# Kernel optimization log

Hardware: AMD Instinct MI355X
Metric: run time of the kernel (lower is better)

The kernel has to match this reference:

```python
import jax, jax.numpy as jnp
import numpy as np

N = 100000          # nodes
E = 1600000         # directed edges
B = 64              # graphs in the batch
IN_D, HID, OUT_D = 20, 128, 256
EPS = 1e-5


def setup_inputs() -> dict:
    key = jax.random.key(0)
    ks = jax.random.split(key, 16)
    x = jax.random.normal(ks[0], (N, IN_D), dtype=jnp.float32)
    edge_index = jax.random.randint(ks[1], (2, E), 0, N, dtype=jnp.int64)
    batch = jnp.sort(jax.random.randint(ks[2], (N,), 0, B, dtype=jnp.int64))

    def lin(k, fi, fo):
        kw, kb = jax.random.split(k)
        s = 1.0 / np.sqrt(fi)
        W = jax.random.uniform(kw, (fi, fo), jnp.float32, -s, s)
        b = jax.random.uniform(kb, (fo,), jnp.float32, -s, s)
        return W, b

    W1, b1 = lin(ks[3], IN_D, HID)
    W2, b2 = lin(ks[4], HID, HID)
    W3, b3 = lin(ks[5], HID, OUT_D)
    res_W, res_b = lin(ks[6], IN_D, HID)
    return {
        "x": x, "edge_index": edge_index, "batch": batch,
        "W1": W1, "b1": b1, "W2": W2, "b2": b2, "W3": W3, "b3": b3,
        "res_W": res_W, "res_b": res_b,
        "ln1_g": jnp.ones((HID,), jnp.float32), "ln1_b": jnp.zeros((HID,), jnp.float32),
        "ln2_g": jnp.ones((HID,), jnp.float32), "ln2_b": jnp.zeros((HID,), jnp.float32),
    }


def layer_norm(h, g, b):
    mu = jnp.mean(h, axis=-1, keepdims=True)
    var = jnp.mean((h - mu) ** 2, axis=-1, keepdims=True)
    return (h - mu) * jax.lax.rsqrt(var + EPS) * g + b


def gcn_conv(h, W, b, src, dst, norm):
    # h: [N, Fi] -> transform then normalized scatter-sum over edges (incl. self-loops)
    h = h @ W                                  # [N, Fo]
    msg = h[src] * norm[:, None]               # [E+N, Fo] gather
    out = jax.ops.segment_sum(msg, dst, num_segments=N)  # scatter
    return out + b


def reference(x, edge_index, batch, W1, b1, W2, b2, W3, b3, res_W, res_b,
              ln1_g, ln1_b, ln2_g, ln2_b):
    loops = jnp.arange(N, dtype=edge_index.dtype)
    src = jnp.concatenate([edge_index[0], loops])
    dst = jnp.concatenate([edge_index[1], loops])
    # symmetric GCN normalization (degrees include self-loops, so deg >= 1)
    deg = jax.ops.segment_sum(jnp.ones_like(dst, jnp.float32), dst, num_segments=N)
    dinv = jax.lax.rsqrt(deg)
    norm = dinv[src] * dinv[dst]               # [E+N]

    residual = x @ res_W + res_b
    h = gcn_conv(x, W1, b1, src, dst, norm)
    h = jax.nn.relu(layer_norm(h + residual, ln1_g, ln1_b))
    residual2 = h
    h = gcn_conv(h, W2, b2, src, dst, norm)
    h = jax.nn.relu(layer_norm(h + residual2, ln2_g, ln2_b))
    h = gcn_conv(h, W3, b3, src, dst, norm)    # [N, 256]

    # global mean pool per graph
    cnt = jax.ops.segment_sum(jnp.ones((N,), jnp.float32), batch, num_segments=B)
    pooled = jax.ops.segment_sum(h, batch, num_segments=B) / jnp.maximum(cnt, 1.0)[:, None]
    return pooled                              # [B, 256]
```

## Files before the change

kernel.cpp:

```cpp
#include <hip/hip_runtime.h>
#include <hip/hip_bf16.h>
#include <hip/hip_fp16.h>
#include <hip/hip_fp8.h>


typedef unsigned short ushort_t;
typedef unsigned int uint_t;
typedef __attribute__((ext_vector_type(8))) short bf16x8;
typedef __attribute__((ext_vector_type(4))) float f32x4;
typedef __attribute__((ext_vector_type(2))) float f32x2;

constexpr int N  = 100000;
constexpr int E  = 1600000;
constexpr int B  = 64;
constexpr int IND = 20;
constexpr int HID = 128;
constexpr int OUTD = 256;

constexpr int NBUK = (N + 127) / 128;
constexpr int GB   = 256;
constexpr int EPB  = E / GB;
constexpr int BMAX = 3072;

__device__ inline ushort_t f2bf(float f) {
  union { float f; uint_t u; } v; v.f = f;
  uint_t r = v.u + 0x7fffu + ((v.u >> 16) & 1u);
  return (ushort_t)(r >> 16);
}
__device__ inline float bflo(uint_t u) { return __uint_as_float(u << 16); }
__device__ inline float bfhi(uint_t u) { return __uint_as_float(u & 0xffff0000u); }

__device__ inline uint_t pkbf(float a, float b) {
  uint_t r;
  asm("v_cvt_pk_bf16_f32 %0, %1, %2" : "=v"(r) : "v"(a), "v"(b));
  return r;
}

#if defined(__has_builtin)
#if __has_builtin(__builtin_amdgcn_cvt_f32_fp8) && __has_builtin(__builtin_amdgcn_cvt_pk_fp8_f32)
#define FP8_HW 1
#endif
#if __has_builtin(__builtin_amdgcn_cvt_pk_f32_fp8)
#define FP8_PK 1
#endif
#endif

template <int S>
__device__ inline float fp8dec(uint_t u) {
#ifdef FP8_HW
  return __builtin_amdgcn_cvt_f32_fp8(u, S);
#else
  __hip_fp8_storage_t b = (__hip_fp8_storage_t)((u >> (8 * S)) & 0xffu);
  __half_raw hr = __hip_cvt_fp8_to_halfraw(b, __HIP_E4M3);
  return __half2float(*(__half*)&hr);
#endif
}

template <int W>
__device__ inline f32x2 fp8dec2(uint_t u) {
#ifdef FP8_PK
  return __builtin_amdgcn_cvt_pk_f32_fp8(u, W != 0);
#else
  f32x2 r; r.x = fp8dec<W * 2>(u); r.y = fp8dec<W * 2 + 1>(u); return r;
#endif
}

template <bool W>
__device__ inline uint_t fp8pk2(float a, float b, uint_t old) {
#ifdef FP8_HW
  return __builtin_amdgcn_cvt_pk_fp8_f32(a, b, old, W);
#else
  uint_t lo = (uint_t)__hip_cvt_float_to_fp8(a, __HIP_SATFINITE, __HIP_E4M3);
  uint_t hi = (uint_t)__hip_cvt_float_to_fp8(b, __HIP_SATFINITE, __HIP_E4M3);
  uint_t pair = lo | (hi << 8);
  return W ? ((old & 0x0000ffffu) | (pair << 16)) : ((old & 0xffff0000u) | pair);
#endif
}

__device__ inline uint_t fp8pair2bf(uint_t b0, uint_t b1) {
#ifdef FP8_PK
  f32x2 f = fp8dec2<0>(b0 | (b1 << 8));
  return pkbf(f.x, f.y);
#else
  return (uint_t)f2bf(fp8dec<0>(b0)) | ((uint_t)f2bf(fp8dec<0>(b1)) << 16);
#endif
}


__global__ __launch_bounds__(256) void k_prep(const int* __restrict__ eidx,
                                              int* __restrict__ histd,
                                              int* __restrict__ hists,
                                              const float* __restrict__ W2,
                                              const float* __restrict__ W1,
                                              const float* __restrict__ resW,
                                              ushort_t* __restrict__ wpack,
                                              ushort_t* __restrict__ w1pack,
                                              const int* __restrict__ batch,
                                              int* __restrict__ starts) {
  const int bid = blockIdx.x;
  if (bid < GB) {
    __shared__ int hd[NBUK], hs[NBUK];
    for (int i = threadIdx.x; i < NBUK; i += 256) { hd[i] = 0; hs[i] = 0; }
    __syncthreads();
    const long base = (long)bid * EPB;
    for (int i = threadIdx.x; i < EPB; i += 256) {
      atomicAdd(&hs[eidx[base + i] >> 7], 1);
      atomicAdd(&hd[eidx[E + base + i] >> 7], 1);
    }
    __syncthreads();
    for (int i = threadIdx.x; i < NBUK; i += 256) {
      histd[(long)bid * NBUK + i] = hd[i];
      hists[(long)bid * NBUK + i] = hs[i];
    }
  } else if (bid < GB + 96) {
    int idx = (bid - GB) * 256 + threadIdx.x;
    if (idx < 16384) {
      int j = idx & 7, L = (idx >> 3) & 63, kt = (idx >> 9) & 3, t = idx >> 11;
      int k = kt * 32 + ((L >> 4) & 3) * 8 + j;
      int n = t * 16 + (L & 15);
      wpack[idx] = f2bf(W2[k * HID + n]);
    } else {
      int i2 = idx - 16384;
      int j = i2 & 7, L = (i2 >> 3) & 63, kt = (i2 >> 9) & 1, t = i2 >> 10;
      int k = kt * 32 + ((L >> 4) & 3) * 8 + j;
      int n = t * 16 + (L & 15);
      float v = 0.f;
      if (k < IND) v = W1[k * HID + n];
      else if (k >= 32 && k < 32 + IND) v = resW[(k - 32) * HID + n];
      w1pack[i2] = f2bf(v);
    }
  } else {
    int i = (bid - GB - 96) * 256 + threadIdx.x;
    if (i >= N) return;
    int b = batch[i];
    int prev = (i == 0) ? -1 : batch[i - 1];
    for (int g = prev + 1; g <= b; ++g) starts[g] = i;
    if (i == N - 1)
      for (int g = b + 1; g <= B; ++g) starts[g] = N;
  }
}


__global__ __launch_bounds__(256) void k_bscan2x(int* __restrict__ histd,
                                                 int* __restrict__ btd,
                                                 int* __restrict__ hists,
                                                 int* __restrict__ bts) {
  __shared__ int s[256];
  const int which = (blockIdx.x >= NBUK);
  const int j = which ? blockIdx.x - NBUK : blockIdx.x;
  int* hist = which ? hists : histd;
  int* btotal = which ? bts : btd;
  const int tid = threadIdx.x;
  int v = hist[(long)tid * NBUK + j];
  s[tid] = v;
  for (int off = 1; off < 256; off <<= 1) {
    __syncthreads();
    int x = (tid >= off) ? s[tid - off] : 0;
    __syncthreads();
    s[tid] += x;
  }
  hist[(long)tid * NBUK + j] = s[tid] - v;
  if (tid == 255) btotal[j] = s[255];
}

__global__ __launch_bounds__(256) void k_bktscan2x(const int* __restrict__ btd,
                                                   int* __restrict__ bexcl,
                                                   const int* __restrict__ bts,
                                                   int* __restrict__ bexcl2,
                                                   int* __restrict__ rowptr) {
  __shared__ int s[256];
  const int* bt = blockIdx.x ? bts : btd;
  int* bx = blockIdx.x ? bexcl2 : bexcl;
  int tid = threadIdx.x;
  int base = tid * 4;
  int v0 = (base + 0 < NBUK) ? bt[base + 0] : 0;
  int v1 = (base + 1 < NBUK) ? bt[base + 1] : 0;
  int v2 = (base + 2 < NBUK) ? bt[base + 2] : 0;
  int v3 = (base + 3 < NBUK) ? bt[base + 3] : 0;
  int p0 = v0, p1 = p0 + v1, p2 = p1 + v2, p3 = p2 + v3;
  s[tid] = p3;
  for (int off = 1; off < 256; off <<= 1) {
    __syncthreads();
    int x = (tid >= off) ? s[tid - off] : 0;
    __syncthreads();
    s[tid] += x;
  }
  int excl = s[tid] - p3;
  if (base + 0 < NBUK) bx[base + 1] = excl + p0;
  if (base + 1 < NBUK) bx[base + 2] = excl + p1;
  if (base + 2 < NBUK) bx[base + 3] = excl + p2;
  if (base + 3 < NBUK) bx[base + 4] = excl + p3;
  if (tid == 0) { bx[0] = 0; if (blockIdx.x == 0) rowptr[N] = E; }
}

__global__ __launch_bounds__(1024) void k_scatter(const int* __restrict__ eidx,
                                                  const int* __restrict__ histd,
                                                  const int* __restrict__ bexcl,
                                                  const int* __restrict__ hists,
                                                  const int* __restrict__ bexcl2,
                                                  int* __restrict__ ebuf,
                                                  int* __restrict__ ebuf2) {
  __shared__ int hd[NBUK], hs[NBUK];
  const int l = ((blockIdx.x & 7) << 5) + (blockIdx.x >> 3);
  const long hrow = (long)l * NBUK;
  for (int i = threadIdx.x; i < NBUK; i += 1024) {
    hd[i] = bexcl[i] + histd[hrow + i];
    hs[i] = bexcl2[i] + hists[hrow + i];
  }
  __syncthreads();
  const long base = (long)l * EPB;
  for (int i = threadIdx.x; i < EPB; i += 1024) {
    int s = eidx[base + i];
    int d = eidx[E + base + i];
    int pos = atomicAdd(&hd[d >> 7], 1);
    ebuf[pos] = s | ((d & 127) << 20);
    int pos2 = atomicAdd(&hs[s >> 7], 1);
    ebuf2[pos2] = ((s & 127) << 17) | d;
  }
}

__global__ __launch_bounds__(256) void k_csr(const int* __restrict__ ebuf,
                                             const int* __restrict__ bexcl,
                                             const float* __restrict__ x,
                                             int* __restrict__ rowptr,
                                             float* __restrict__ dinv,
                                             int* __restrict__ colsrc,
                                             ushort_t* __restrict__ xs16) {
  __shared__ int deg[128], s[128], cur[128];
  __shared__ float dv[128];
  __shared__ int lout[BMAX];
  const int j = blockIdx.x, tid = threadIdx.x;
  const int e0 = bexcl[j], e1 = bexcl[j + 1];
  const int cnt = e1 - e0;
  if (tid < 128) deg[tid] = 0;
  __syncthreads();
  for (int i = tid; i < cnt; i += 256)
    atomicAdd(&deg[(ebuf[e0 + i] >> 20) & 127], 1);
  __syncthreads();
  int v = (tid < 128) ? deg[tid] : 0;
  if (tid < 128) s[tid] = v;
  for (int off = 1; off < 128; off <<= 1) {
    __syncthreads();
    int x2 = (tid < 128 && tid >= off) ? s[tid - off] : 0;
    __syncthreads();
    if (tid < 128) s[tid] += x2;
  }
  __syncthreads();
  if (tid < 128) {
    int ex = s[tid] - v;
    cur[tid] = ex;
    float d = rsqrtf((float)(1 + v));
    dv[tid] = d;
    int node = j * 128 + tid;
    if (node < N) {
      rowptr[node] = e0 + ex;
      dinv[node] = d;
    }
  }
  __syncthreads();
  if (cnt <= BMAX) {
    for (int i = tid; i < cnt; i += 256) {
      int p = ebuf[e0 + i];
      int pos = atomicAdd(&cur[(p >> 20) & 127], 1);
      lout[pos] = p & 0xFFFFF;
    }
    __syncthreads();
    for (int i = tid; i < cnt; i += 256) colsrc[e0 + i] = lout[i];
  } else {
    for (int i = tid; i < cnt; i += 256) {
      int p = ebuf[e0 + i];
      int pos = atomicAdd(&cur[(p >> 20) & 127], 1);
      colsrc[e0 + pos] = p & 0xFFFFF;
    }
  }
  for (int idx = tid; idx < 128 * IND; idx += 256) {
    int n = idx / IND;
    long node = (long)j * 128 + n;
    if (node < N)
      xs16[node * IND + idx % IND] = f2bf(x[node * IND + idx % IND] * dv[n]);
  }
}


constexpr int ASTR = 72;
constexpr int CSTR = 132;

__global__ __launch_bounds__(256) void k_layer1(const ushort_t* __restrict__ xs16,
                                                const float* __restrict__ x,
                                                const int* __restrict__ rowptr,
                                                const int* __restrict__ colsrc,
                                                const ushort_t* __restrict__ w1pack,
                                                const float* __restrict__ b1,
                                                const float* __restrict__ resb,
                                                const float* __restrict__ g1,
                                                const float* __restrict__ bb1,
                                                const float* __restrict__ dinv,
                                                unsigned char* __restrict__ h8a) {
  __shared__ ushort_t A[16 * ASTR];
  __shared__ float Cs[16 * CSTR];
  const int tid = threadIdx.x;
  const long node0 = (long)blockIdx.x * 16;
  for (int idx = tid; idx < 16 * ASTR; idx += 256) A[idx] = 0;
  __syncthreads();
  for (int idx = tid; idx < 16 * IND; idx += 256) {
    int n = idx / IND, k = idx % IND;
    A[n * ASTR + 32 + k] = f2bf(x[(node0 + n) * IND + k]);
  }
  if (tid < 160) {
    int n = tid / 10, cc = (tid % 10) * 2;
    long i = node0 + n;
    float di = dinv[i];
    uint_t u = *(const uint_t*)(xs16 + i * IND + cc);
    float a0 = bflo(u), a1 = bfhi(u);
    int e0 = rowptr[i], e1 = rowptr[i + 1];
#pragma unroll 4
    for (int e = e0; e < e1; ++e) {
      int s = colsrc[e];
      uint_t v = *(const uint_t*)(xs16 + (long)s * IND + cc);
      a0 += bflo(v); a1 += bfhi(v);
    }
    *(uint_t*)&A[n * ASTR + cc] = pkbf(a0 * di, a1 * di);
  }
  __syncthreads();
  const int lane = tid & 63, w = tid >> 6;
  {
    const int arow = lane & 15, aq = lane >> 4;
    f32x4 acc0 = {0.f, 0.f, 0.f, 0.f}, acc1 = {0.f, 0.f, 0.f, 0.f};
    const int t0 = w * 2, t1 = t0 + 1;
#pragma unroll
    for (int kt = 0; kt < 2; ++kt) {
      bf16x8 af = *(const bf16x8*)&A[arow * ASTR + kt * 32 + aq * 8];
      bf16x8 b0 = *(const bf16x8*)&w1pack[(t0 * 2 + kt) * 512 + lane * 8];
      bf16x8 b1f = *(const bf16x8*)&w1pack[(t1 * 2 + kt) * 512 + lane * 8];
      acc0 = __builtin_amdgcn_mfma_f32_16x16x32_bf16(af, b0, acc0, 0, 0, 0);
      acc1 = __builtin_amdgcn_mfma_f32_16x16x32_bf16(af, b1f, acc1, 0, 0, 0);
    }
#pragma unroll
    for (int r = 0; r < 4; ++r) {
      Cs[(aq * 4 + r) * CSTR + t0 * 16 + arow] = acc0[r];
      Cs[(aq * 4 + r) * CSTR + t1 * 16 + arow] = acc1[r];
    }
  }
  __syncthreads();
  const int nidx = tid >> 5, col = (tid & 31) * 4;
  float4 bz = *(const float4*)&b1[col];
  float4 rz = *(const float4*)&resb[col];
  bz.x += rz.x; bz.y += rz.y; bz.z += rz.z; bz.w += rz.w;
  float4 gz = *(const float4*)&g1[col];
  float4 bbz = *(const float4*)&bb1[col];
#pragma unroll
  for (int m = 0; m < 2; ++m) {
    int nl = nidx + m * 8;
    long nm = node0 + nl;
    float4 o = *(const float4*)&Cs[nl * CSTR + col];
    o.x += bz.x; o.y += bz.y; o.z += bz.z; o.w += bz.w;
    float s = o.x + o.y + o.z + o.w;
    float q = o.x * o.x + o.y * o.y + o.z * o.z + o.w * o.w;
#pragma unroll
    for (int off = 1; off <= 16; off <<= 1) {
      s += __shfl_xor(s, off);
      q += __shfl_xor(q, off);
    }
    float mu = s * (1.f / 128.f);
    float var = q * (1.f / 128.f) - mu * mu;
    float rs = rsqrtf(var + 1e-5f);
    float y0 = fmaxf(fmaf((o.x - mu) * rs, gz.x, bbz.x), 0.f);
    float y1 = fmaxf(fmaf((o.y - mu) * rs, gz.y, bbz.y), 0.f);
    float y2 = fmaxf(fmaf((o.z - mu) * rs, gz.z, bbz.z), 0.f);
    float y3 = fmaxf(fmaf((o.w - mu) * rs, gz.w, bbz.w), 0.f);
    float di = dinv[nm];
    uint_t p = fp8pk2<false>(y0 * di, y1 * di, 0u);
    p = fp8pk2<true>(y2 * di, y3 * di, p);
    *(uint_t*)&h8a[nm * HID + col] = p;
  }
}


constexpr int XSTR = 136;

__global__ __launch_bounds__(256) void k_layer2(const unsigned char* __restrict__ h8a,
                                                const float* __restrict__ dinv,
                                                const int* __restrict__ rowptr,
                                                const int* __restrict__ colsrc,
                                                const ushort_t* __restrict__ wpack,
                                                const float* __restrict__ bias,
                                                const float* __restrict__ g2,
                                                const float* __restrict__ bb2,
                                                unsigned char* __restrict__ h8b) {
  __shared__ ushort_t XsB[16 * XSTR];
  __shared__ float Cs[16 * CSTR];
  const int tid = threadIdx.x;
  const long node0 = (long)blockIdx.x * 16;
  const int lane = tid & 63, w = tid >> 6;
  {
    const int grp = lane >> 4, l16 = lane & 15, c8 = l16 * 8;
    const long i = node0 + w * 4 + grp;
    const float di = dinv[i];
    f32x2 a0, a1, a2, a3;
    {
      uint2 u = *(const uint2*)(h8a + i * HID + c8);
      a0 = fp8dec2<0>(u.x); a1 = fp8dec2<1>(u.x);
      a2 = fp8dec2<0>(u.y); a3 = fp8dec2<1>(u.y);
    }
    const int e0 = rowptr[i], e1 = rowptr[i + 1];
#pragma unroll 4
    for (int e = e0; e < e1; ++e) {
      int s = colsrc[e];
      uint2 u = *(const uint2*)(h8a + (long)s * HID + c8);
      a0 += fp8dec2<0>(u.x); a1 += fp8dec2<1>(u.x);
      a2 += fp8dec2<0>(u.y); a3 += fp8dec2<1>(u.y);
    }
    uint_t p0 = pkbf(a0.x * di, a0.y * di);
    uint_t p1 = pkbf(a1.x * di, a1.y * di);
    uint_t p2 = pkbf(a2.x * di, a2.y * di);
    uint_t p3 = pkbf(a3.x * di, a3.y * di);
    *(uint4*)&XsB[(w * 4 + grp) * XSTR + c8] = make_uint4(p0, p1, p2, p3);
  }
  __syncthreads();
  {
    const int arow = lane & 15, aq = lane >> 4;
    f32x4 acc0 = {0.f, 0.f, 0.f, 0.f}, acc1 = {0.f, 0.f, 0.f, 0.f};
    const int t0 = w * 2, t1 = w * 2 + 1;
#pragma unroll
    for (int kt = 0; kt < 4; ++kt) {
      bf16x8 af = *(const bf16x8*)&XsB[arow * XSTR + kt * 32 + aq * 8];
      bf16x8 b0 = *(const bf16x8*)&wpack[(t0 * 4 + kt) * 512 + lane * 8];
      bf16x8 b1 = *(const bf16x8*)&wpack[(t1 * 4 + kt) * 512 + lane * 8];
      acc0 = __builtin_amdgcn_mfma_f32_16x16x32_bf16(af, b0, acc0, 0, 0, 0);
      acc1 = __builtin_amdgcn_mfma_f32_16x16x32_bf16(af, b1, acc1, 0, 0, 0);
    }
#pragma unroll
    for (int r = 0; r < 4; ++r) {
      Cs[(aq * 4 + r) * CSTR + t0 * 16 + arow] = acc0[r];
      Cs[(aq * 4 + r) * CSTR + t1 * 16 + arow] = acc1[r];
    }
  }
  __syncthreads();
  const int nidx = tid >> 5;
  const int col = (tid & 31) * 4;
  float4 bz = *(const float4*)&bias[col];
  float4 gz = *(const float4*)&g2[col];
  float4 bbz = *(const float4*)&bb2[col];
#pragma unroll
  for (int m = 0; m < 2; ++m) {
    int nl = nidx + m * 8;
    long nm = node0 + nl;
    float di = dinv[nm];
    float rdi = 1.0f / di;
    uint_t ur = *(const uint_t*)&h8a[nm * HID + col];
    f32x2 r01 = fp8dec2<0>(ur), r23 = fp8dec2<1>(ur);
    float4 o = *(const float4*)&Cs[nl * CSTR + col];
    o.x += bz.x + r01.x * rdi;
    o.y += bz.y + r01.y * rdi;
    o.z += bz.z + r23.x * rdi;
    o.w += bz.w + r23.y * rdi;
    float s = o.x + o.y + o.z + o.w;
    float q = o.x * o.x + o.y * o.y + o.z * o.z + o.w * o.w;
#pragma unroll
    for (int off = 1; off <= 16; off <<= 1) {
      s += __shfl_xor(s, off);
      q += __shfl_xor(q, off);
    }
    float mu = s * (1.f / 128.f);
    float var = q * (1.f / 128.f) - mu * mu;
    float rs = rsqrtf(var + 1e-5f);
    float y0 = fmaxf(fmaf((o.x - mu) * rs, gz.x, bbz.x), 0.f);
    float y1 = fmaxf(fmaf((o.y - mu) * rs, gz.y, bbz.y), 0.f);
    float y2 = fmaxf(fmaf((o.z - mu) * rs, gz.z, bbz.z), 0.f);
    float y3 = fmaxf(fmaf((o.w - mu) * rs, gz.w, bbz.w), 0.f);
    uint_t p = fp8pk2<false>(y0 * di, y1 * di, 0u);
    p = fp8pk2<true>(y2 * di, y3 * di, p);
    *(uint_t*)&h8b[nm * HID + col] = p;
  }
}


constexpr int RSTR8 = 136;
constexpr int CP    = 132;

__global__ __launch_bounds__(256) void k_pool3m(const unsigned char* __restrict__ h8b,
                                                const int* __restrict__ bexcl2,
                                                const int* __restrict__ ebuf2,
                                                const int* __restrict__ batch,
                                                const float* __restrict__ dinv,
                                                ushort_t* __restrict__ partial) {
  __shared__ float Cm[B * CP];
  __shared__ unsigned char R8[128 * RSTR8];
  const int j = blockIdx.x, tid = threadIdx.x;
  const long nbase = (long)j * 128;
  const int validRows = min(128, N - (int)nbase);
  for (int i = tid; i < B * CP; i += 256) Cm[i] = 0.f;
  for (int i = tid; i < 128 * (HID / 16); i += 256) {
    int s = i >> 3;
    int ch = (i & 7) * 16;
    uint4 pk = make_uint4(0u, 0u, 0u, 0u);
    if (s < validRows)
      pk = *(const uint4*)(h8b + (nbase + s) * HID + ch);
    *(uint4*)&R8[s * RSTR8 + ch] = pk;
  }
  __syncthreads();
  const int e0 = bexcl2[j], e1 = bexcl2[j + 1];
  for (int e = e0 + tid; e < e1; e += 256) {
    int p = ebuf2[e];
    int s = (p >> 17) & 127;
    int d = p & 0x1FFFF;
    atomicAdd(&Cm[batch[d] * CP + s], dinv[d]);
  }
  for (int n = tid; n < validRows; n += 256) {
    long node = nbase + n;
    atomicAdd(&Cm[batch[node] * CP + n], dinv[node]);
  }
  __syncthreads();
  const int lane = tid & 63, wid = tid >> 6;
  const int m16 = lane & 15, quad = lane >> 4;
  f32x4 acc[4][2];
#pragma unroll
  for (int mt = 0; mt < 4; ++mt)
#pragma unroll
    for (int ntl = 0; ntl < 2; ++ntl) acc[mt][ntl] = (f32x4){0.f, 0.f, 0.f, 0.f};
#pragma unroll
  for (int kt = 0; kt < 4; ++kt) {
    union { uint_t p[4]; bf16x8 v; } bf[2];
#pragma unroll
    for (int ntl = 0; ntl < 2; ++ntl) {
      int nt = wid * 2 + ntl;
#pragma unroll
      for (int jj = 0; jj < 8; jj += 2) {
        uint_t byte0 = R8[(kt * 32 + quad * 8 + jj) * RSTR8 + nt * 16 + m16];
        uint_t byte1 = R8[(kt * 32 + quad * 8 + jj + 1) * RSTR8 + nt * 16 + m16];
        bf[ntl].p[jj >> 1] = fp8pair2bf(byte0, byte1);
      }
    }
#pragma unroll
    for (int mt = 0; mt < 4; ++mt) {
      float4 c0 = *(const float4*)&Cm[(mt * 16 + m16) * CP + kt * 32 + quad * 8];
      float4 c1 = *(const float4*)&Cm[(mt * 16 + m16) * CP + kt * 32 + quad * 8 + 4];
      union { uint_t p[4]; bf16x8 v; } af;
      af.p[0] = pkbf(c0.x, c0.y); af.p[1] = pkbf(c0.z, c0.w);
      af.p[2] = pkbf(c1.x, c1.y); af.p[3] = pkbf(c1.z, c1.w);
      acc[mt][0] = __builtin_amdgcn_mfma_f32_16x16x32_bf16(af.v, bf[0].v, acc[mt][0], 0, 0, 0);
      acc[mt][1] = __builtin_amdgcn_mfma_f32_16x16x32_bf16(af.v, bf[1].v, acc[mt][1], 0, 0, 0);
    }
  }
  ushort_t* slab = partial + (long)j * (B * HID);
#pragma unroll
  for (int mt = 0; mt < 4; ++mt)
#pragma unroll
    for (int ntl = 0; ntl < 2; ++ntl)
#pragma unroll
      for (int r = 0; r < 4; ++r) {
        int g = mt * 16 + quad * 4 + r;
        int ch = (wid * 2 + ntl) * 16 + m16;
        slab[g * HID + ch] = f2bf(acc[mt][ntl][r]);
      }
}

__global__ __launch_bounds__(256) void k_pool_reduce(const ushort_t* __restrict__ partial,
                                                     float* __restrict__ pooled) {
  __shared__ float s[4][64];
  const int tid = threadIdx.x;
  const int ol = tid & 7, jl = tid >> 3;
  const int o0 = blockIdx.x * 64 + ol * 8;
  float a0 = 0.f, a1 = 0.f, a2 = 0.f, a3 = 0.f,
        a4 = 0.f, a5 = 0.f, a6 = 0.f, a7 = 0.f;
#pragma unroll 2
  for (int j = jl; j < NBUK; j += 32) {
    uint4 v = *(const uint4*)&partial[(long)j * (B * HID) + o0];
    a0 += bflo(v.x); a1 += bfhi(v.x);
    a2 += bflo(v.y); a3 += bfhi(v.y);
    a4 += bflo(v.z); a5 += bfhi(v.z);
    a6 += bflo(v.w); a7 += bfhi(v.w);
  }
#pragma unroll
  for (int off = 8; off <= 32; off <<= 1) {
    a0 += __shfl_xor(a0, off); a1 += __shfl_xor(a1, off);
    a2 += __shfl_xor(a2, off); a3 += __shfl_xor(a3, off);
    a4 += __shfl_xor(a4, off); a5 += __shfl_xor(a5, off);
    a6 += __shfl_xor(a6, off); a7 += __shfl_xor(a7, off);
  }
  const int w = tid >> 6, lane = tid & 63;
  if (lane < 8) {
    float* d = &s[w][lane * 8];
    d[0] = a0; d[1] = a1; d[2] = a2; d[3] = a3;
    d[4] = a4; d[5] = a5; d[6] = a6; d[7] = a7;
  }
  __syncthreads();
  if (tid < 64)
    pooled[blockIdx.x * 64 + tid] = s[0][tid] + s[1][tid] + s[2][tid] + s[3][tid];
}


__global__ __launch_bounds__(256) void k_final(const float* __restrict__ pooled,
                                               const int* __restrict__ starts,
                                               const float* __restrict__ W3,
                                               const float* __restrict__ b3,
                                               float* __restrict__ out) {
  __shared__ float p[HID];
  int g = blockIdx.x, tid = threadIdx.x;
  int len = starts[g + 1] - starts[g];
  float scale = 1.0f / fmaxf((float)len, 1.0f);
  if (tid < HID) p[tid] = pooled[g * HID + tid] * scale;
  __syncthreads();
  float a = b3[tid];
  for (int k = 0; k < HID; ++k) a = fmaf(p[k], W3[k * OUTD + tid], a);
  out[g * OUTD + tid] = a;
}


extern "C" void kernel_launch(void* const* d_in, const int* in_sizes, int n_in,
                              void* d_out, int out_size, void* d_ws, size_t ws_size,
                              hipStream_t stream) {
  const float* x    = (const float*)d_in[0];
  const int*   eidx = (const int*)d_in[1];
  const int*   batch= (const int*)d_in[2];
  const float* W1   = (const float*)d_in[3];
  const float* b1   = (const float*)d_in[4];
  const float* W2   = (const float*)d_in[5];
  const float* b2   = (const float*)d_in[6];
  const float* W3   = (const float*)d_in[7];
  const float* b3   = (const float*)d_in[8];
  const float* resW = (const float*)d_in[9];
  const float* resb = (const float*)d_in[10];
  const float* g1   = (const float*)d_in[11];
  const float* bb1  = (const float*)d_in[12];
  const float* g2   = (const float*)d_in[13];
  const float* bb2  = (const float*)d_in[14];
  float* out = (float*)d_out;

  char* w = (char*)d_ws;
  size_t off = 0;
  auto alloc = [&](size_t bytes) {
    char* p = w + off;
    off = (off + bytes + 1023) & ~(size_t)1023;
    return p;
  };
  float* dinv   = (float*)alloc((size_t)N * 4);
  int*   rowptr = (int*)alloc((size_t)(N + 1) * 4);
  int*   colsrc = (int*)alloc((size_t)E * 4);
  int*   ebuf   = (int*)alloc((size_t)E * 4);
  int*   ebuf2  = (int*)alloc((size_t)E * 4);
  int*   hist   = (int*)alloc((size_t)GB * NBUK * 4);
  int*   hist2  = (int*)alloc((size_t)GB * NBUK * 4);
  int*   btotal = (int*)alloc((size_t)NBUK * 4);
  int*   btotal2= (int*)alloc((size_t)NBUK * 4);
  int*   bexcl  = (int*)alloc((size_t)(NBUK + 1) * 4);
  int*   bexcl2 = (int*)alloc((size_t)(NBUK + 1) * 4);
  int*   starts = (int*)alloc((size_t)(B + 1) * 4);
  float* pooled = (float*)alloc((size_t)B * HID * 4);
  ushort_t* xs16   = (ushort_t*)alloc((size_t)N * IND * 2);
  ushort_t* wpack  = (ushort_t*)alloc((size_t)HID * HID * 2);
  ushort_t* w1pack = (ushort_t*)alloc((size_t)8192 * 2);
  unsigned char* h8a = (unsigned char*)alloc((size_t)N * HID);
  unsigned char* h8b = (unsigned char*)alloc((size_t)N * HID);
  ushort_t* partial = (ushort_t*)alloc((size_t)NBUK * B * HID * 2);

  k_prep<<<GB + 96 + (N + 255) / 256, 256, 0, stream>>>(
      eidx, hist, hist2, W2, W1, resW, wpack, w1pack, batch, starts);
  k_bscan2x<<<2 * NBUK, 256, 0, stream>>>(hist, btotal, hist2, btotal2);
  k_bktscan2x<<<2, 256, 0, stream>>>(btotal, bexcl, btotal2, bexcl2, rowptr);
  k_scatter<<<GB, 1024, 0, stream>>>(eidx, hist, bexcl, hist2, bexcl2, ebuf, ebuf2);
  k_csr<<<NBUK, 256, 0, stream>>>(ebuf, bexcl, x, rowptr, dinv, colsrc, xs16);

  k_layer1<<<N / 16, 256, 0, stream>>>(xs16, x, rowptr, colsrc, w1pack,
                                       b1, resb, g1, bb1, dinv, h8a);

  k_layer2<<<N / 16, 256, 0, stream>>>(h8a, dinv, rowptr, colsrc,
                                       wpack, b2, g2, bb2, h8b);

  k_pool3m<<<NBUK, 256, 0, stream>>>(h8b, bexcl2, ebuf2, batch, dinv, partial);
  k_pool_reduce<<<(B * HID) / 64, 256, 0, stream>>>(partial, pooled);
  k_final<<<B, 256, 0, stream>>>(pooled, starts, W3, b3, out);
}
```

Before: 260.3 us.

## Stage scatter through shared memory for coalesced bucketed global writes

The edge scatter kernel now does two passes (dst-bucketed and src-bucketed). Each pass builds a local histogram, runs a block-wide scan and places the entries into a shared-memory staging buffer in bucket order. It then writes them out contiguously per bucket, replacing scattered per-edge global stores. This aims to improve write coalescing, at the cost of extra passes over the edge list, many barriers and a large shared-memory footprint (about 38KB) that limits occupancy.

```diff
diff --git a/kernel.cpp b/kernel.cpp
--- a/kernel.cpp
+++ b/kernel.cpp
@@ -200,22 +200,63 @@
                                                   const int* __restrict__ bexcl2,
                                                   int* __restrict__ ebuf,
                                                   int* __restrict__ ebuf2) {
-  __shared__ int hd[NBUK], hs[NBUK];
+  __shared__ int lhist[NBUK];
+  __shared__ int lscan[NBUK];
+  __shared__ int gbase[NBUK];
+  __shared__ int stmp[1024];
+  __shared__ int staged[EPB];
+  __shared__ ushort_t sbuk[EPB];
+  const int tid = threadIdx.x;
   const int l = ((blockIdx.x & 7) << 5) + (blockIdx.x >> 3);
   const long hrow = (long)l * NBUK;
-  for (int i = threadIdx.x; i < NBUK; i += 1024) {
-    hd[i] = bexcl[i] + histd[hrow + i];
-    hs[i] = bexcl2[i] + hists[hrow + i];
-  }
-  __syncthreads();
   const long base = (long)l * EPB;
-  for (int i = threadIdx.x; i < EPB; i += 1024) {
-    int s = eidx[base + i];
-    int d = eidx[E + base + i];
-    int pos = atomicAdd(&hd[d >> 7], 1);
-    ebuf[pos] = s | ((d & 127) << 20);
-    int pos2 = atomicAdd(&hs[s >> 7], 1);
-    ebuf2[pos2] = ((s & 127) << 17) | d;
+
+#pragma unroll
+  for (int pass = 0; pass < 2; ++pass) {
+    const int* hist = pass ? hists : histd;
+    const int* bx = pass ? bexcl2 : bexcl;
+    int* out = pass ? ebuf2 : ebuf;
+    for (int i = tid; i < NBUK; i += 1024) {
+      lhist[i] = 0;
+      gbase[i] = bx[i] + hist[hrow + i];
+    }
+    __syncthreads();
+    for (int i = tid; i < EPB; i += 1024) {
+      int key = eidx[(pass ? 0 : E) + base + i];
+      atomicAdd(&lhist[key >> 7], 1);
+    }
+    __syncthreads();
+    {
+      int v = (tid < NBUK) ? lhist[tid] : 0;
+      stmp[tid] = v;
+      for (int off = 1; off < 1024; off <<= 1) {
+        __syncthreads();
+        int x2 = (tid >= off) ? stmp[tid - off] : 0;
+        __syncthreads();
+        stmp[tid] += x2;
+      }
+      __syncthreads();
+      if (tid < NBUK) {
+        int ex = stmp[tid] - v;
+        lscan[tid] = ex;
+        lhist[tid] = ex;
+      }
+    }
+    __syncthreads();
+    for (int i = tid; i < EPB; i += 1024) {
+      int s = eidx[base + i];
+      int d = eidx[E + base + i];
+      int b = (pass ? s : d) >> 7;
+      int pos = atomicAdd(&lhist[b], 1);
+      staged[pos] = pass ? (((s & 127) << 17) | d) : (s | ((d & 127) << 20));
+      sbuk[pos] = (ushort_t)b;
+    }
+    __syncthreads();
+    for (int i = tid; i < EPB; i += 1024) {
+      int b = sbuk[i];
+      out[gbase[b] + (i - lscan[b])] = staged[i];
+    }
+    __syncthreads();
   }
 }
 
```

Result: no change. 258.3 us, median of 2 (-0.8%).
